# Kernel tuning notes

Measured on AMD Instinct MI355X. Metric: run time of the kernel, lower is better.

Reference implementation:

```python
import jax, jax.numpy as jnp
import numpy as np

B, S, C, H = 4096, 31, 512, 8  # seq_len fixed at num_particles+1 = 31 by the module
HD = C // H
EPS = 1e-5


def setup_inputs() -> dict:
    key = jax.random.key(0)
    ks = jax.random.split(key, 10)
    rn = lambda k, sh: jax.random.normal(k, sh, dtype=jnp.float32)
    scale = 1.0 / np.sqrt(C)
    return {
        "x": rn(ks[0], (B, S, C)),
        "norm_w": 1.0 + 0.1 * rn(ks[1], (C,)),
        "norm_b": 0.1 * rn(ks[2], (C,)),
        "Wq": rn(ks[3], (C, C)) * scale,
        "Wk": rn(ks[4], (C, C)) * scale,
        "Wv": rn(ks[5], (C, C)) * scale,
        "Wout": rn(ks[6], (C, C)) * scale,
        "b_out": 0.1 * rn(ks[7], (C,)),
        "pen_w": 1.0 + 0.1 * rn(ks[8], (S * S,)),
        "pen_b": 0.1 * rn(ks[9], (S * S,)),
    }


def reference(x, norm_w, norm_b, Wq, Wk, Wv, Wout, b_out, pen_w, pen_b):
    # BatchNorm1d(in_dim) applied to x.transpose(1,2): per-channel stats over (batch, seq).
    # Training-mode BN: biased variance, eps=1e-5.
    mu = jnp.mean(x, axis=(0, 1))
    var = jnp.var(x, axis=(0, 1))
    xn = (x - mu) * jax.lax.rsqrt(var + EPS) * norm_w + norm_b

    # QKV projections (Linear, no bias): y = x @ W.T
    q = (xn @ Wq.T).reshape(B, S, H, HD)
    k = (xn @ Wk.T).reshape(B, S, H, HD)
    v = (xn @ Wv.T).reshape(B, S, H, HD)

    # energy: [B, H, S, S]
    energy = jnp.einsum("nqhc,nkhc->nhqk", q, k)

    # BatchNorm1d(S*S) on energy.view(B,H,S*S).transpose(1,2):
    # per-(q,k)-position stats over (batch, heads).
    mu2 = jnp.mean(energy, axis=(0, 1))   # [S, S]
    var2 = jnp.var(energy, axis=(0, 1))   # [S, S]
    en = (energy - mu2) * jax.lax.rsqrt(var2 + EPS)
    en = en * pen_w.reshape(S, S) + pen_b.reshape(S, S)

    attn = jax.nn.softmax(en / jnp.sqrt(jnp.float32(C)), axis=-1)

    out = jnp.einsum("nhql,nlhc->nqhc", attn, v).reshape(B, S, C)
    return out @ Wout.T + b_out + x
```

## Files before the change

kernel.cpp:

```cpp
#include <hip/hip_runtime.h>

typedef unsigned short u16;
typedef unsigned int   u32;
typedef __attribute__((ext_vector_type(4))) float f32x4;
typedef __attribute__((ext_vector_type(8))) short bf16x8;

#define BB 4096
#define SS 31
#define CC 512
#define HH 8
#define MM (BB*SS)
#define SSQ (SS*SS)

__device__ __forceinline__ u16 f2bf(float f){
  union { float f; u32 u; } v; v.f = f;
  u32 r = (v.u + 0x7fffu + ((v.u >> 16) & 1u)) >> 16;
  return (u16)r;
}
__device__ __forceinline__ float bf2f(u16 u){
  union { u32 u; float f; } v; v.u = ((u32)u) << 16;
  return v.f;
}
__device__ __forceinline__ void gload_lds16(const u16* g, u16* l){
  __builtin_amdgcn_global_load_lds((const __attribute__((address_space(1))) void*)g,
                                   (__attribute__((address_space(3))) void*)l, 16, 0, 0);
}

__global__ __launch_bounds__(512) void bn1_stats_k(const float* __restrict__ x, float* __restrict__ acc){
  int c = threadIdx.x;
  float s = 0.f, q = 0.f;
  for (int r = blockIdx.x; r < MM; r += gridDim.x){
    float v = x[(long)r*CC + c];
    s += v; q += v*v;
  }
  atomicAdd(&acc[c], s);
  atomicAdd(&acc[CC + c], q);
}

__global__ __launch_bounds__(512) void bn1_final_k(const float* __restrict__ acc, const float* __restrict__ w,
                                                   const float* __restrict__ b, float* __restrict__ scsh){
  int c = threadIdx.x;
  const float invN = 1.f / (float)MM;
  float mu  = acc[c] * invN;
  float var = acc[CC+c] * invN - mu*mu;
  float rs  = rsqrtf(var + 1e-5f);
  float sc  = w[c] * rs;
  scsh[c]    = sc;
  scsh[CC+c] = b[c] - mu*sc;
}

__global__ __launch_bounds__(256) void bn1_apply_k(const float* __restrict__ x, const float* __restrict__ scsh,
                                                   u16* __restrict__ xn){
  const int tot = MM*CC/8;
  int stride = gridDim.x * blockDim.x;
  for (int i = blockIdx.x*blockDim.x + threadIdx.x; i < tot; i += stride){
    const f32x4* xp = (const f32x4*)x;
    f32x4 a = xp[2l*i], b2 = xp[2l*i+1];
    int c = (i*8) & (CC-1);
    u16 r[8];
    #pragma unroll
    for (int j = 0; j < 4; j++) r[j]   = f2bf(a[j] *scsh[c+j]   + scsh[CC+c+j]);
    #pragma unroll
    for (int j = 0; j < 4; j++) r[4+j] = f2bf(b2[j]*scsh[c+4+j] + scsh[CC+c+4+j]);
    *(bf16x8*)(xn + 8l*i) = *(bf16x8*)r;
  }
}

__global__ __launch_bounds__(256) void wconv_k(const float* __restrict__ a, const float* __restrict__ b,
                                               const float* __restrict__ c, const float* __restrict__ d,
                                               u16* __restrict__ o){
  int i = blockIdx.x*256 + threadIdx.x;
  if (i >= 4*CC*CC) return;
  int w = i >> 18;
  const float* src = w==0 ? a : (w==1 ? b : (w==2 ? c : d));
  o[i] = f2bf(src[i & (CC*CC-1)]);
}

template<int FINAL>
__global__ __launch_bounds__(512,2) void gemm256_k(
    const u16* __restrict__ A,
    const u16* __restrict__ W0, const u16* __restrict__ W1, const u16* __restrict__ W2,
    u16* __restrict__ O0, u16* __restrict__ O1, u16* __restrict__ O2,
    const float* __restrict__ bias, const float* __restrict__ resid, float* __restrict__ out)
{
  __shared__ u16 lds[3*16384];
  const int t  = threadIdx.x;
  const int mt = blockIdx.y * 256;
  int nt; const u16* Wsel; u16* Osel = nullptr;
  if (FINAL) { Wsel = W0; nt = blockIdx.x; }
  else {
    int wi = blockIdx.x >> 1; nt = blockIdx.x & 1;
    Wsel = wi==0 ? W0 : (wi==1 ? W1 : W2);
    Osel = wi==0 ? O0 : (wi==1 ? O1 : O2);
  }
  const u16* Ab = A    + (long)mt*CC;
  const u16* Bb = Wsel + (long)nt*256*CC;
  const int lane = t & 63;
  const int wv = t >> 6, wm = wv >> 2, wn = wv & 3;
  const int lr = lane & 15, hi = lane >> 4;
  const int srow = t >> 2;
  const int sc   = t & 3;
  const int sg   = sc ^ ((t >> 3) & 3);

  f32x4 acc[8][4];
  #pragma unroll
  for (int m=0;m<8;m++)
    #pragma unroll
    for (int n=0;n<4;n++)
      acc[m][n] = (f32x4){0.f,0.f,0.f,0.f};

  auto STAGE = [&](int kt){
    u16* Al = &lds[(kt % 3) * 16384];
    u16* Bl = Al + 8192;
    const u16* As = Ab + (long)srow*CC + kt*32 + sg*8;
    const u16* Bs = Bb + (long)srow*CC + kt*32 + sg*8;
    gload_lds16(As,          &Al[srow*32 + sc*8]);
    gload_lds16(As + 128*CC, &Al[(srow+128)*32 + sc*8]);
    gload_lds16(Bs,          &Bl[srow*32 + sc*8]);
    gload_lds16(Bs + 128*CC, &Bl[(srow+128)*32 + sc*8]);
  };

  STAGE(0); STAGE(1);
  asm volatile("s_waitcnt vmcnt(4)" ::: "memory");
  asm volatile("s_barrier" ::: "memory");

  const int chR = hi ^ ((lr >> 1) & 3);
  #pragma unroll 1
  for (int kt = 0; kt < 16; ++kt){
    if (kt < 14) STAGE(kt + 2);
    const u16* Al = &lds[(kt % 3) * 16384];
    const u16* Bl = Al + 8192;
    bf16x8 af[8], bfr[4];
    #pragma unroll
    for (int m=0;m<8;m++){
      int row = wm*128 + m*16 + lr;
      af[m] = *(const bf16x8*)&Al[row*32 + chR*8];
    }
    #pragma unroll
    for (int n=0;n<4;n++){
      int row = wn*64 + n*16 + lr;
      bfr[n] = *(const bf16x8*)&Bl[row*32 + chR*8];
    }
    asm volatile("s_waitcnt lgkmcnt(0)" ::: "memory");
    __builtin_amdgcn_sched_barrier(0);
    __builtin_amdgcn_s_setprio(1);
    #pragma unroll
    for (int m=0;m<8;m++)
      #pragma unroll
      for (int n=0;n<4;n++)
        acc[m][n] = __builtin_amdgcn_mfma_f32_16x16x32_bf16(af[m], bfr[n], acc[m][n], 0, 0, 0);
    __builtin_amdgcn_s_setprio(0);
    if (kt < 14)       asm volatile("s_waitcnt vmcnt(4)" ::: "memory");
    else if (kt == 14) asm volatile("s_waitcnt vmcnt(0)" ::: "memory");
    if (kt < 15)       asm volatile("s_barrier" ::: "memory");
  }

  #pragma unroll
  for (int m=0;m<8;m++){
    int gr = mt + wm*128 + m*16 + hi*4;
    #pragma unroll
    for (int n=0;n<4;n++){
      int gc = nt*256 + wn*64 + n*16 + lr;
      #pragma unroll
      for (int j=0;j<4;j++){
        long off = (long)(gr + j)*CC + gc;
        if (FINAL) out[off] = acc[m][n][j] + bias[gc] + resid[off];
        else       Osel[off] = f2bf(acc[m][n][j]);
      }
    }
  }
}

__global__ __launch_bounds__(256) void energy_k(const u16* __restrict__ q, const u16* __restrict__ k,
                                                float* __restrict__ e){
  const int wv = threadIdx.x >> 6, lane = threadIdx.x & 63;
  const int lr = lane & 15, hi = lane >> 4;
  #pragma unroll 1
  for (int it = 0; it < 4; it++){
    int p = blockIdx.x*4 + wv + 8192*it;
    int b = p >> 3, h = p & 7;
    long base = ((long)b*SS)*CC + h*64;
    bf16x8 aq[2][2], ak[2][2];
    #pragma unroll
    for (int m=0;m<2;m++){
      int s = m*16 + lr;
      #pragma unroll
      for (int ks=0;ks<2;ks++){
        bf16x8 z = {0,0,0,0,0,0,0,0};
        aq[m][ks] = z; ak[m][ks] = z;
        if (s < SS){
          aq[m][ks] = *(const bf16x8*)&q[base + (long)s*CC + ks*32 + hi*8];
          ak[m][ks] = *(const bf16x8*)&k[base + (long)s*CC + ks*32 + hi*8];
        }
      }
    }
    f32x4 acc[2][2];
    #pragma unroll
    for (int m=0;m<2;m++)
      #pragma unroll
      for (int n=0;n<2;n++)
        acc[m][n] = (f32x4){0.f,0.f,0.f,0.f};
    #pragma unroll
    for (int ks=0;ks<2;ks++)
      #pragma unroll
      for (int m=0;m<2;m++)
        #pragma unroll
        for (int n=0;n<2;n++)
          acc[m][n] = __builtin_amdgcn_mfma_f32_16x16x32_bf16(aq[m][ks], ak[n][ks], acc[m][n], 0, 0, 0);
    long eb = (long)p*SSQ;
    #pragma unroll
    for (int m=0;m<2;m++)
      #pragma unroll
      for (int n=0;n<2;n++)
        #pragma unroll
        for (int j=0;j<4;j++){
          int s = m*16 + hi*4 + j, s2 = n*16 + lr;
          if (s < SS && s2 < SS) e[eb + s*SS + s2] = acc[m][n][j];
        }
  }
}

__global__ __launch_bounds__(256) void bn2_stats_k(const float* __restrict__ e, float* __restrict__ acc2){
  int p = blockIdx.x*256 + threadIdx.x;
  if (p >= SSQ) return;
  float s = 0.f, q = 0.f;
  int r0 = blockIdx.y * 128;
  for (int r = r0; r < r0 + 128; r++){
    float v = e[(long)r*SSQ + p];
    s += v; q += v*v;
  }
  atomicAdd(&acc2[p], s);
  atomicAdd(&acc2[1024 + p], q);
}

__global__ __launch_bounds__(256) void bn2_final_k(const float* __restrict__ acc2, const float* __restrict__ pw,
                                                   const float* __restrict__ pb, float* __restrict__ ss2){
  int p = blockIdx.x*256 + threadIdx.x;
  if (p >= SSQ) return;
  const float invN = 1.f/32768.f;
  const float invs = 0.04419417382415922f;
  float mu  = acc2[p]*invN;
  float var = acc2[1024+p]*invN - mu*mu;
  float rs  = rsqrtf(var + 1e-5f);
  float srp = rs * pw[p];
  ss2[p]      = srp * invs;
  ss2[1024+p] = (pb[p] - mu*srp) * invs;
}

__global__ __launch_bounds__(256) void attn_pv_k(const float* __restrict__ e, const float* __restrict__ ss2,
                                                 const u16* __restrict__ v, u16* __restrict__ ctx){
  __shared__ float sc2[SSQ], sh2[SSQ];
  __shared__ float att[4][SSQ];
  for (int i = threadIdx.x; i < SSQ; i += 256){ sc2[i] = ss2[i]; sh2[i] = ss2[1024+i]; }
  __syncthreads();
  const int wv = threadIdx.x >> 6, lane = threadIdx.x & 63;
  #pragma unroll 1
  for (int it = 0; it < 4; it++){
    int p = blockIdx.x*4 + wv + 8192*it;
    int b = p >> 3, h = p & 7;
    long eb = (long)p*SSQ;
    for (int i = lane; i < SSQ; i += 64)
      att[wv][i] = e[eb + i]*sc2[i] + sh2[i];
    __syncthreads();
    if (lane < SS){
      int ro = lane*SS;
      float mx = -1e30f;
      for (int j=0;j<SS;j++) mx = fmaxf(mx, att[wv][ro + j]);
      float sum = 0.f;
      for (int j=0;j<SS;j++) sum += __expf(att[wv][ro + j] - mx);
      float inv = 1.f / sum;
      for (int j=0;j<SS;j++) att[wv][ro + j] = __expf(att[wv][ro + j] - mx) * inv;
    }
    __syncthreads();
    long vbase = ((long)b*SS)*CC + h*64 + lane;
    float vr[SS];
    #pragma unroll
    for (int j=0;j<SS;j++) vr[j] = bf2f(v[vbase + (long)j*CC]);
    #pragma unroll 1
    for (int s=0;s<SS;s++){
      float c = 0.f;
      #pragma unroll
      for (int j=0;j<SS;j++) c += att[wv][s*SS + j] * vr[j];
      ctx[vbase + (long)s*CC] = f2bf(c);
    }
    __syncthreads();
  }
}

extern "C" void kernel_launch(void* const* d_in, const int* in_sizes, int n_in,
                              void* d_out, int out_size, void* d_ws, size_t ws_size,
                              hipStream_t stream)
{
  const float* x      = (const float*)d_in[0];
  const float* norm_w = (const float*)d_in[1];
  const float* norm_b = (const float*)d_in[2];
  const float* Wq     = (const float*)d_in[3];
  const float* Wk     = (const float*)d_in[4];
  const float* Wv     = (const float*)d_in[5];
  const float* Wout   = (const float*)d_in[6];
  const float* b_out  = (const float*)d_in[7];
  const float* pen_w  = (const float*)d_in[8];
  const float* pen_b  = (const float*)d_in[9];
  float* out = (float*)d_out;

  char* ws = (char*)d_ws;
  const size_t WQB   = 0;
  const size_t STATS = 2097152;
  const size_t SCSH1 = STATS + 16384;
  const size_t SS2O  = SCSH1 + 4096;
  const size_t BIG0  = 2129920;
  const size_t BIGSZ = 130023424;
  u16*   wq    = (u16*)(ws + WQB);
  float* stats = (float*)(ws + STATS);
  float* acc2  = (float*)(ws + STATS + 4096);
  float* scsh  = (float*)(ws + SCSH1);
  float* ss2   = (float*)(ws + SS2O);
  u16*   xn    = (u16*)(ws + BIG0);
  float* e     = (float*)(ws + BIG0);
  u16*   qb    = (u16*)(ws + BIG0 + BIGSZ);
  u16*   kb    = (u16*)(ws + BIG0 + 2*BIGSZ);
  u16*   vb    = (u16*)(ws + BIG0 + 3*BIGSZ);
  u16*   ctx   = qb;

  (void)hipMemsetAsync(ws + STATS, 0, 16384, stream);
  wconv_k<<<4096, 256, 0, stream>>>(Wq, Wk, Wv, Wout, wq);
  bn1_stats_k<<<512, 512, 0, stream>>>(x, stats);
  bn1_final_k<<<1, 512, 0, stream>>>(stats, norm_w, norm_b, scsh);
  bn1_apply_k<<<2048, 256, 0, stream>>>(x, scsh, xn);
  gemm256_k<0><<<dim3(6, 496), 512, 0, stream>>>(xn, wq, wq + 262144, wq + 2*262144,
                                                 qb, kb, vb, nullptr, nullptr, nullptr);
  energy_k<<<2048, 256, 0, stream>>>(qb, kb, e);
  bn2_stats_k<<<dim3(4, 256), 256, 0, stream>>>(e, acc2);
  bn2_final_k<<<4, 256, 0, stream>>>(acc2, pen_w, pen_b, ss2);
  attn_pv_k<<<2048, 256, 0, stream>>>(e, ss2, vb, ctx);
  gemm256_k<1><<<dim3(2, 496), 512, 0, stream>>>(ctx, wq + 3*262144, nullptr, nullptr,
                                                 nullptr, nullptr, nullptr, b_out, x, out);
}
```

Baseline: 1.235 ms.

## Double-buffer GEMM with BK=64, swizzle grid, vectorize BN stats, split softmax rows

The GEMM now uses a two-stage LDS pipeline with a K-tile of 64 instead of a three-stage pipeline with 32, which halves the number of barriers. It also remaps block indices so blocks running at the same time share A and B tiles in L2. Separately, the BN1 stats kernel uses float4 loads with a shared-memory reduction before the atomics. The softmax in attn_pv splits each row across two lanes joined by shuffles. The trade-off is that the shallower pipeline waits for vmcnt(0) every iteration, which may expose more memory latency.

```diff
diff --git a/kernel.cpp b/kernel.cpp
--- a/kernel.cpp
+++ b/kernel.cpp
@@ -26,15 +26,28 @@
                                    (__attribute__((address_space(3))) void*)l, 16, 0, 0);
 }
 
-__global__ __launch_bounds__(512) void bn1_stats_k(const float* __restrict__ x, float* __restrict__ acc){
-  int c = threadIdx.x;
-  float s = 0.f, q = 0.f;
-  for (int r = blockIdx.x; r < MM; r += gridDim.x){
-    float v = x[(long)r*CC + c];
+__global__ __launch_bounds__(256) void bn1_stats_k(const float* __restrict__ x, float* __restrict__ acc){
+  const int t = threadIdx.x;
+  const int c = (t & 127) * 4;
+  const int rof = t >> 7;
+  f32x4 s = (f32x4){0.f,0.f,0.f,0.f}, q = (f32x4){0.f,0.f,0.f,0.f};
+  for (int r = blockIdx.x*2 + rof; r < MM; r += gridDim.x*2){
+    f32x4 v = *(const f32x4*)(x + (long)r*CC + c);
     s += v; q += v*v;
   }
-  atomicAdd(&acc[c], s);
-  atomicAdd(&acc[CC + c], q);
+  __shared__ f32x4 red[256][2];
+  red[t][0] = s; red[t][1] = q;
+  __syncthreads();
+  if (t < 128){
+    s = red[t][0] + red[t+128][0];
+    q = red[t][1] + red[t+128][1];
+    int c0 = t*4;
+    #pragma unroll
+    for (int j=0;j<4;j++){
+      atomicAdd(&acc[c0+j], s[j]);
+      atomicAdd(&acc[CC+c0+j], q[j]);
+    }
+  }
 }
 
 __global__ __launch_bounds__(512) void bn1_final_k(const float* __restrict__ acc, const float* __restrict__ w,
@@ -77,19 +90,25 @@
 }
 
 template<int FINAL>
-__global__ __launch_bounds__(512,2) void gemm256_k(
+__global__ __launch_bounds__(512,2) void gemm2p_k(
     const u16* __restrict__ A,
     const u16* __restrict__ W0, const u16* __restrict__ W1, const u16* __restrict__ W2,
     u16* __restrict__ O0, u16* __restrict__ O1, u16* __restrict__ O2,
     const float* __restrict__ bias, const float* __restrict__ resid, float* __restrict__ out)
 {
-  __shared__ u16 lds[3*16384];
-  const int t  = threadIdx.x;
-  const int mt = blockIdx.y * 256;
+  __shared__ u16 lds[2*32768];
+  const int NTX = FINAL ? 2 : 6;
+  const int CH  = FINAL ? 124 : 372;
+  int lin = blockIdx.x + NTX*blockIdx.y;
+  int swz = (lin & 7)*CH + (lin >> 3);
+  int bx = swz % NTX, by = swz / NTX;
+
+  const int t = threadIdx.x;
+  const int mt = by * 256;
   int nt; const u16* Wsel; u16* Osel = nullptr;
-  if (FINAL) { Wsel = W0; nt = blockIdx.x; }
+  if (FINAL) { Wsel = W0; nt = bx; }
   else {
-    int wi = blockIdx.x >> 1; nt = blockIdx.x & 1;
+    int wi = bx >> 1; nt = bx & 1;
     Wsel = wi==0 ? W0 : (wi==1 ? W1 : W2);
     Osel = wi==0 ? O0 : (wi==1 ? O1 : O2);
   }
@@ -98,9 +117,9 @@
   const int lane = t & 63;
   const int wv = t >> 6, wm = wv >> 2, wn = wv & 3;
   const int lr = lane & 15, hi = lane >> 4;
-  const int srow = t >> 2;
-  const int sc   = t & 3;
-  const int sg   = sc ^ ((t >> 3) & 3);
+  const int srow = t >> 3;
+  const int sc   = t & 7;
+  const int sg   = sc ^ ((t >> 4) & 7);
 
   f32x4 acc[8][4];
   #pragma unroll
@@ -110,49 +129,59 @@
       acc[m][n] = (f32x4){0.f,0.f,0.f,0.f};
 
   auto STAGE = [&](int kt){
-    u16* Al = &lds[(kt % 3) * 16384];
-    u16* Bl = Al + 8192;
-    const u16* As = Ab + (long)srow*CC + kt*32 + sg*8;
-    const u16* Bs = Bb + (long)srow*CC + kt*32 + sg*8;
-    gload_lds16(As,          &Al[srow*32 + sc*8]);
-    gload_lds16(As + 128*CC, &Al[(srow+128)*32 + sc*8]);
-    gload_lds16(Bs,          &Bl[srow*32 + sc*8]);
-    gload_lds16(Bs + 128*CC, &Bl[(srow+128)*32 + sc*8]);
+    u16* dst = &lds[(kt & 1) * 32768];
+    const u16* As = Ab + kt*64 + sg*8;
+    const u16* Bs = Bb + kt*64 + sg*8;
+    #pragma unroll
+    for (int u=0;u<4;u++){
+      int r = srow + 64*u;
+      gload_lds16(As + (long)r*CC, &dst[r*64 + sc*8]);
+    }
+    #pragma unroll
+    for (int u=0;u<4;u++){
+      int r = srow + 64*u;
+      gload_lds16(Bs + (long)r*CC, &dst[16384 + r*64 + sc*8]);
+    }
   };
 
-  STAGE(0); STAGE(1);
-  asm volatile("s_waitcnt vmcnt(4)" ::: "memory");
+  STAGE(0);
+  asm volatile("s_waitcnt vmcnt(0)" ::: "memory");
   asm volatile("s_barrier" ::: "memory");
 
-  const int chR = hi ^ ((lr >> 1) & 3);
+  const int rsw = (lr >> 1) & 7;
   #pragma unroll 1
-  for (int kt = 0; kt < 16; ++kt){
-    if (kt < 14) STAGE(kt + 2);
-    const u16* Al = &lds[(kt % 3) * 16384];
-    const u16* Bl = Al + 8192;
-    bf16x8 af[8], bfr[4];
-    #pragma unroll
-    for (int m=0;m<8;m++){
-      int row = wm*128 + m*16 + lr;
-      af[m] = *(const bf16x8*)&Al[row*32 + chR*8];
-    }
-    #pragma unroll
-    for (int n=0;n<4;n++){
-      int row = wn*64 + n*16 + lr;
-      bfr[n] = *(const bf16x8*)&Bl[row*32 + chR*8];
-    }
-    asm volatile("s_waitcnt lgkmcnt(0)" ::: "memory");
-    __builtin_amdgcn_sched_barrier(0);
-    __builtin_amdgcn_s_setprio(1);
-    #pragma unroll
-    for (int m=0;m<8;m++)
-      #pragma unroll
-      for (int n=0;n<4;n++)
-        acc[m][n] = __builtin_amdgcn_mfma_f32_16x16x32_bf16(af[m], bfr[n], acc[m][n], 0, 0, 0);
-    __builtin_amdgcn_s_setprio(0);
-    if (kt < 14)       asm volatile("s_waitcnt vmcnt(4)" ::: "memory");
-    else if (kt == 14) asm volatile("s_waitcnt vmcnt(0)" ::: "memory");
-    if (kt < 15)       asm volatile("s_barrier" ::: "memory");
+  for (int kt = 0; kt < 8; ++kt){
+    if (kt < 7) STAGE(kt + 1);
+    const u16* Al = &lds[(kt & 1) * 32768];
+    const u16* Bl = Al + 16384;
+    #pragma unroll
+    for (int ks = 0; ks < 2; ++ks){
+      const int ch = (ks*4 + hi) ^ rsw;
+      bf16x8 af[8], bfr[4];
+      #pragma unroll
+      for (int m=0;m<8;m++){
+        int row = wm*128 + m*16 + lr;
+        af[m] = *(const bf16x8*)&Al[row*64 + ch*8];
+      }
+      #pragma unroll
+      for (int n=0;n<4;n++){
+        int row = wn*64 + n*16 + lr;
+        bfr[n] = *(const bf16x8*)&Bl[row*64 + ch*8];
+      }
+      asm volatile("s_waitcnt lgkmcnt(0)" ::: "memory");
+      __builtin_amdgcn_sched_barrier(0);
+      __builtin_amdgcn_s_setprio(1);
+      #pragma unroll
+      for (int m=0;m<8;m++)
+        #pragma unroll
+        for (int n=0;n<4;n++)
+          acc[m][n] = __builtin_amdgcn_mfma_f32_16x16x32_bf16(af[m], bfr[n], acc[m][n], 0, 0, 0);
+      __builtin_amdgcn_s_setprio(0);
+    }
+    if (kt < 7){
+      asm volatile("s_waitcnt vmcnt(0)" ::: "memory");
+      asm volatile("s_barrier" ::: "memory");
+    }
   }
 
   #pragma unroll
@@ -262,14 +291,20 @@
     for (int i = lane; i < SSQ; i += 64)
       att[wv][i] = e[eb + i]*sc2[i] + sh2[i];
     __syncthreads();
-    if (lane < SS){
-      int ro = lane*SS;
-      float mx = -1e30f;
-      for (int j=0;j<SS;j++) mx = fmaxf(mx, att[wv][ro + j]);
-      float sum = 0.f;
-      for (int j=0;j<SS;j++) sum += __expf(att[wv][ro + j] - mx);
-      float inv = 1.f / sum;
-      for (int j=0;j<SS;j++) att[wv][ro + j] = __expf(att[wv][ro + j] - mx) * inv;
+    {
+      int r = lane >> 1, half = lane & 1;
+      if (r < SS){
+        int ro = r*SS;
+        int j0 = half*16, j1 = half ? SS : 16;
+        float mx = -1e30f;
+        for (int j=j0;j<j1;j++) mx = fmaxf(mx, att[wv][ro + j]);
+        mx = fmaxf(mx, __shfl_xor(mx, 1));
+        float sum = 0.f;
+        for (int j=j0;j<j1;j++) sum += __expf(att[wv][ro + j] - mx);
+        sum += __shfl_xor(sum, 1);
+        float inv = 1.f / sum;
+        for (int j=j0;j<j1;j++) att[wv][ro + j] = __expf(att[wv][ro + j] - mx) * inv;
+      }
     }
     __syncthreads();
     long vbase = ((long)b*SS)*CC + h*64 + lane;
@@ -324,15 +359,15 @@
 
   (void)hipMemsetAsync(ws + STATS, 0, 16384, stream);
   wconv_k<<<4096, 256, 0, stream>>>(Wq, Wk, Wv, Wout, wq);
-  bn1_stats_k<<<512, 512, 0, stream>>>(x, stats);
+  bn1_stats_k<<<512, 256, 0, stream>>>(x, stats);
   bn1_final_k<<<1, 512, 0, stream>>>(stats, norm_w, norm_b, scsh);
   bn1_apply_k<<<2048, 256, 0, stream>>>(x, scsh, xn);
-  gemm256_k<0><<<dim3(6, 496), 512, 0, stream>>>(xn, wq, wq + 262144, wq + 2*262144,
-                                                 qb, kb, vb, nullptr, nullptr, nullptr);
+  gemm2p_k<0><<<dim3(6, 496), 512, 0, stream>>>(xn, wq, wq + 262144, wq + 2*262144,
+                                                qb, kb, vb, nullptr, nullptr, nullptr);
   energy_k<<<2048, 256, 0, stream>>>(qb, kb, e);
   bn2_stats_k<<<dim3(4, 256), 256, 0, stream>>>(e, acc2);
   bn2_final_k<<<4, 256, 0, stream>>>(acc2, pen_w, pen_b, ss2);
   attn_pv_k<<<2048, 256, 0, stream>>>(e, ss2, vb, ctx);
-  gemm256_k<1><<<dim3(2, 496), 512, 0, stream>>>(ctx, wq + 3*262144, nullptr, nullptr,
-                                                 nullptr, nullptr, nullptr, b_out, x, out);
-}
+  gemm2p_k<1><<<dim3(2, 496), 512, 0, stream>>>(ctx, wq + 3*262144, nullptr, nullptr,
+                                                nullptr, nullptr, nullptr, b_out, x, out);
+}
```

New measurement: 1.214 ms. Within noise of the previous version (-1.7%).
